# Kernel tuning notes

Measured on AMD Instinct MI355X. Metric: run time of the kernel, lower is better.

Reference implementation:

```python
import jax, jax.numpy as jnp
import numpy as np

NUM_FEATURES = 129  # lstm_hidden + 1
GAMMA = 1.0


def _lstm(x, W_ih, W_hh, b_ih, b_hh):
    # x: [B,S,F]; W_ih: [4H,F]; W_hh: [4H,H]; gates in torch order i,f,g,o
    B, S, _ = x.shape
    H = W_hh.shape[1]
    xg = jnp.einsum('bsf,gf->bsg', x, W_ih) + b_ih  # [B,S,4H]

    def step(carry, xt):
        h, c = carry
        g = xt + h @ W_hh.T + b_hh
        i, f, gg, o = jnp.split(g, 4, axis=-1)
        c = jax.nn.sigmoid(f) * c + jax.nn.sigmoid(i) * jnp.tanh(gg)
        h = jax.nn.sigmoid(o) * jnp.tanh(c)
        return (h, c), h

    h0 = jnp.zeros((B, H), x.dtype)
    (_, _), hs = jax.lax.scan(step, (h0, h0), jnp.swapaxes(xg, 0, 1))
    return jnp.swapaxes(hs, 0, 1)  # [B,S,H]


def setup_inputs() -> dict:
    key = jax.random.key(0)
    ks = jax.random.split(key, 10)
    B, S, F, H = 16, 2048, 129, 128
    s = 0.05  # keep activations in a sane range
    return {
        'x': jax.random.normal(ks[0], (B, S, F), jnp.float32),
        'prototypes': jax.random.normal(ks[1], (B, S, F), jnp.float32),
        'W_ih': jax.random.normal(ks[2], (4 * H, F), jnp.float32) * s,
        'W_hh': jax.random.normal(ks[3], (4 * H, H), jnp.float32) * s,
        'b_ih': jax.random.normal(ks[4], (4 * H,), jnp.float32) * s,
        'b_hh': jax.random.normal(ks[5], (4 * H,), jnp.float32) * s,
        'Wc': jax.random.normal(ks[6], (4, F, F), jnp.float32) * s,
        'bc': jax.random.normal(ks[7], (4, F), jnp.float32) * s,
        'Wh': jax.random.normal(ks[8], (2, F), jnp.float32) * s,
        'bh': jax.random.normal(ks[9], (2,), jnp.float32) * s,
    }


def reference(x, prototypes, W_ih, W_hh, b_ih, b_hh, Wc, bc, Wh, bh):
    lstm_out = _lstm(x, W_ih, W_hh, b_ih, b_hh)  # [B,S,H]
    # attention path is detached in the original (numpy round-trip)
    q = jax.lax.stop_gradient(lstm_out)
    # note: scale uses num_features (embed_dim of the attention object), not H
    scores = jnp.einsum('bqh,bkh->bqk', q, q) / jnp.sqrt(jnp.float32(NUM_FEATURES))
    attn = jax.nn.softmax(scores, axis=-1)
    context = jnp.einsum('bqk,bkh->bqh', attn, q)  # [B,S,H]
    # vectorized RBF kernel vs prototypes (original does a Python loop per (i,j))
    diff = x - prototypes
    kernel_features = jnp.exp(-GAMMA * jnp.sum(diff * diff, axis=-1, keepdims=True))  # [B,S,1]
    h = jnp.concatenate([context, kernel_features], axis=-1)  # [B,S,NUM_FEATURES]
    for l in range(4):
        h = jax.nn.relu(h @ Wc[l].T + bc[l])
    logits = h @ Wh.T + bh  # [B,S,2]
    return jax.nn.log_softmax(logits, axis=-1)
```

## Files before the change

kernel.cpp:

```cpp
#include <hip/hip_runtime.h>
#include <stdint.h>

#define B_ 16
#define S_ 2048
#define F_ 129
#define H_ 128
#define G_ 512

typedef float f32x4 __attribute__((ext_vector_type(4)));
typedef float f32x4a4 __attribute__((ext_vector_type(4), aligned(4)));
typedef float f32x2 __attribute__((ext_vector_type(2)));
typedef short s16x8 __attribute__((ext_vector_type(8)));
typedef _Float16 f16x8 __attribute__((ext_vector_type(8)));
typedef _Float16 f16x4 __attribute__((ext_vector_type(4)));

#define BAR_LDS() __asm__ volatile("s_waitcnt lgkmcnt(0)\n\ts_barrier" ::: "memory")

__device__ inline unsigned short h2bits(_Float16 h) {
  union { _Float16 h; unsigned short u; } v; v.h = h; return v.u;
}
__device__ inline unsigned short f2h(float f) { return h2bits((_Float16)f); }

__device__ inline float rcp_(float x) { return __builtin_amdgcn_rcpf(x); }

__device__ inline float sigmoid_fast(float x) { return rcp_(1.f + __expf(-x)); }

__device__ inline float tanh_fast(float x) {
  return 1.f - 2.f * rcp_(1.f + __expf(2.f * x));
}

__global__ __launch_bounds__(256) void xg_kernel(const float* __restrict__ x,
    const float* __restrict__ W_ih, const float* __restrict__ b_ih,
    const float* __restrict__ b_hh, _Float16* __restrict__ xg) {
  __shared__ __align__(16) _Float16 xs[64][136];
  __shared__ __align__(16) _Float16 ws[128][136];
  __shared__ float bsum[512];
  int tid = threadIdx.x;
  int lane = tid & 63, w = tid >> 6;
  int l15 = lane & 15, q = lane >> 4;
  long R0 = (long)blockIdx.x * 64;
  for (int it = 0; it < 8; ++it) {
    int i = tid + it * 256;
    int r = i >> 5, cx = (i & 31) * 4;
    f32x4a4 v = *(const f32x4a4*)&x[(R0 + r) * 129 + cx];
    f16x4 hq;
    #pragma unroll
    for (int j = 0; j < 4; ++j) hq[j] = (_Float16)v[j];
    *(f16x4*)&xs[r][cx] = hq;
  }
  if (tid < 64) xs[tid][128] = (_Float16)x[(R0 + tid) * 129 + 128];
  for (int it = 0; it < 2; ++it) {
    int g = tid + it * 256;
    bsum[g] = b_ih[g] + b_hh[g];
  }
  __syncthreads();
  f16x8 Bf[4];
  #pragma unroll
  for (int kb = 0; kb < 4; ++kb)
    Bf[kb] = *(const f16x8*)&xs[16 * w + l15][kb * 32 + q * 8];
  float x128 = (float)xs[16 * w + l15][128];
  f16x4 res[32];
  #pragma unroll
  for (int c = 0; c < 4; ++c) {
    __syncthreads();
    for (int it = 0; it < 16; ++it) {
      int i = tid + it * 256;
      int r = i >> 5, cc = (i & 31) * 4;
      f32x4a4 v = *(const f32x4a4*)&W_ih[(long)(c * 128 + r) * 129 + cc];
      f16x4 hq;
      #pragma unroll
      for (int j = 0; j < 4; ++j) hq[j] = (_Float16)v[j];
      *(f16x4*)&ws[r][cc] = hq;
    }
    if (tid < 128) ws[tid][128] = (_Float16)W_ih[(long)(c * 128 + tid) * 129 + 128];
    __syncthreads();
    #pragma unroll
    for (int t = 0; t < 8; ++t) {
      f32x4 acc;
      acc[0] = 0.f; acc[1] = 0.f; acc[2] = 0.f; acc[3] = 0.f;
      #pragma unroll
      for (int kb = 0; kb < 4; ++kb) {
        f16x8 Af = *(const f16x8*)&ws[t * 16 + l15][kb * 32 + q * 8];
        acc = __builtin_amdgcn_mfma_f32_16x16x32_f16(Af, Bf[kb], acc, 0, 0, 0);
      }
      #pragma unroll
      for (int r = 0; r < 4; ++r) {
        int unit = t * 16 + q * 4 + r;
        float v = acc[r] + bsum[c * 128 + unit] + x128 * (float)ws[unit][128];
        res[t * 4 + r][c] = (_Float16)v;
      }
    }
  }
  long rowbase = (R0 + 16 * w + l15) * G_;
  #pragma unroll
  for (int t = 0; t < 8; ++t)
    #pragma unroll
    for (int r = 0; r < 4; ++r)
      *(f16x4*)&xg[rowbase + (t * 16 + q * 4 + r) * 4] = res[t * 4 + r];
}

__global__ __launch_bounds__(256) void rbf_kernel(const float* __restrict__ x,
    const float* __restrict__ p, float* __restrict__ kf) {
  int wave = threadIdx.x >> 6, lane = threadIdx.x & 63;
  long row = (long)blockIdx.x * 4 + wave;
  const float* xr = x + row * F_;
  const float* pr = p + row * F_;
  float ss = 0.f;
  for (int k = lane; k < F_; k += 64) { float d = xr[k] - pr[k]; ss += d * d; }
  #pragma unroll
  for (int off = 32; off; off >>= 1) ss += __shfl_xor(ss, off, 64);
  if (lane == 0) kf[row] = __expf(-ss);
}

__global__ __launch_bounds__(512, 2) void lstm_kernel(const _Float16* __restrict__ xg,
    const float* __restrict__ W_hh, unsigned short* __restrict__ qbf) {
  __shared__ __align__(16) _Float16 hbuf[2][4 * 144];
  int tid = threadIdx.x;
  int w = tid >> 6, lane = tid & 63;
  int n16 = lane & 15;
  int q8 = lane >> 4;
  int ab = n16 >> 2;
  int u = (w << 4) | n16;
  int bb = blockIdx.x * 4;
  f16x8 Wf[4][4];
  #pragma unroll
  for (int ty = 0; ty < 4; ++ty) {
    #pragma unroll
    for (int kb = 0; kb < 4; ++kb) {
      const float* src = &W_hh[(ty * 128 + u) * H_ + kb * 32 + q8 * 8];
      f16x8 v;
      #pragma unroll
      for (int j = 0; j < 8; ++j) v[j] = (_Float16)src[j];
      Wf[ty][kb] = v;
    }
  }
  for (int i = tid; i < 2 * 4 * 144; i += 512)
    ((_Float16*)hbuf)[i] = (_Float16)0.f;
  float c = 0.f;
  int hoff = ab * 144 + q8 * 8;
  const _Float16* h0 = &hbuf[0][hoff];
  const _Float16* h1 = &hbuf[1][hoff];
  _Float16* hw = &hbuf[0][q8 * 144 + u];
  const int hstride = 4 * 144;
  const _Float16* xb = xg + (long)(bb + q8) * S_ * G_ + u * 4;
  unsigned short* qp = qbf + (long)(bb + q8) * S_ * H_ + u - H_;
  const _Float16* xpf = xb + 4 * G_;
  f16x4 cur[4];
  #pragma unroll
  for (int p = 0; p < 4; ++p) cur[p] = *(const f16x4*)(xb + (long)p * G_);
  unsigned short hvp = 0;
  __syncthreads();
  for (int t = 0; t < S_; t += 4) {
    #pragma unroll
    for (int p = 0; p < 4; ++p) {
      BAR_LDS();
      const _Float16* hsrc = (p & 1) ? h0 : h1;
      f16x8 A[4];
      #pragma unroll
      for (int kb = 0; kb < 4; ++kb)
        A[kb] = *(const f16x8*)(hsrc + kb * 32);
      if (t + p > 0)
        *qp = hvp;
      qp += H_;
      f16x4 xcur = cur[p];
      cur[p] = *(const f16x4*)xpf;
      xpf += G_;
      f32x4 r0a[4], r1a[4];
      #pragma unroll
      for (int ty = 0; ty < 4; ++ty) {
        f32x4 a0, a1;
        a0[0] = (float)xcur[ty]; a0[1] = 0.f; a0[2] = 0.f; a0[3] = 0.f;
        a1[0] = 0.f; a1[1] = 0.f; a1[2] = 0.f; a1[3] = 0.f;
        a0 = __builtin_amdgcn_mfma_f32_16x16x32_f16(A[0], Wf[ty][0], a0, 0, 0, 0);
        a1 = __builtin_amdgcn_mfma_f32_16x16x32_f16(A[2], Wf[ty][2], a1, 0, 0, 0);
        a0 = __builtin_amdgcn_mfma_f32_16x16x32_f16(A[1], Wf[ty][1], a0, 0, 0, 0);
        a1 = __builtin_amdgcn_mfma_f32_16x16x32_f16(A[3], Wf[ty][3], a1, 0, 0, 0);
        r0a[ty] = a0; r1a[ty] = a1;
      }
      float g0 = r0a[0][0] + r1a[0][0];
      float g1 = r0a[1][0] + r1a[1][0];
      float g2 = r0a[2][0] + r1a[2][0];
      float g3 = r0a[3][0] + r1a[3][0];
      float ai = sigmoid_fast(g0);
      float af = sigmoid_fast(g1);
      float ag = tanh_fast(g2);
      float ao = sigmoid_fast(g3);
      c = af * c + ai * ag;
      float hv = ao * tanh_fast(c);
      _Float16 hf = (_Float16)hv;
      hw[(p & 1) * hstride] = hf;
      hvp = h2bits(hf);
    }
  }
  *qp = hvp;
}

__global__ __launch_bounds__(256) void attn_kernel(const unsigned short* __restrict__ qbf,
    float* __restrict__ ctx) {
  __shared__ __align__(16) unsigned short Ks[64 * 136];
  __shared__ __align__(16) unsigned short VT[128 * 72];
  __shared__ __align__(16) unsigned short Ps[4 * 16 * 72];
  int tid = threadIdx.x;
  int lane = tid & 63, w = tid >> 6;
  int b = blockIdx.x >> 5;
  int q0 = (blockIdx.x & 31) * 64;
  const unsigned short* qb = qbf + (long)b * S_ * H_;
  int l15 = lane & 15;
  int koff = (lane >> 4) * 8;
  f16x8 qfrag[4];
  #pragma unroll
  for (int kb = 0; kb < 4; ++kb)
    qfrag[kb] = *(const f16x8*)(qb + (long)(q0 + w * 16 + l15) * H_ + kb * 32 + koff);
  f32x4 oacc[8];
  #pragma unroll
  for (int n = 0; n < 8; ++n)
    #pragma unroll
    for (int r = 0; r < 4; ++r) oacc[n][r] = 0.f;
  float mrow[4], lrow[4];
  #pragma unroll
  for (int r = 0; r < 4; ++r) { mrow[r] = -1e30f; lrow[r] = 0.f; }
  const float scale = 0.08804509063256238f;
  unsigned short* Pw = &Ps[w * 16 * 72];
  for (int t = 0; t < S_ / 64; ++t) {
    {
      int rr = tid >> 4;
      int c0 = (tid & 15) * 8;
      #pragma unroll
      for (int pch = 0; pch < 4; ++pch) {
        int r = pch * 16 + rr;
        s16x8 v = *(const s16x8*)(qb + (long)(t * 64 + r) * H_ + c0);
        *(s16x8*)(&Ks[r * 136 + c0]) = v;
        int rbase = r >> 3, rl = r & 7;
        #pragma unroll
        for (int i = 0; i < 8; ++i) {
          int d = c0 + i;
          VT[d * 72 + ((rbase ^ ((d >> 3) & 7)) << 3) + rl] = (unsigned short)v[i];
        }
      }
    }
    __syncthreads();
    f32x4 sacc[4];
    #pragma unroll
    for (int n = 0; n < 4; ++n) {
      f32x4 acc;
      #pragma unroll
      for (int r = 0; r < 4; ++r) acc[r] = 0.f;
      #pragma unroll
      for (int kb = 0; kb < 4; ++kb) {
        f16x8 bfrag = *(const f16x8*)(&Ks[(n * 16 + l15) * 136 + kb * 32 + koff]);
        acc = __builtin_amdgcn_mfma_f32_16x16x32_f16(qfrag[kb], bfrag, acc, 0, 0, 0);
      }
      sacc[n] = acc;
    }
    #pragma unroll
    for (int r = 0; r < 4; ++r) {
      float mx = fmaxf(fmaxf(sacc[0][r], sacc[1][r]), fmaxf(sacc[2][r], sacc[3][r]));
      #pragma unroll
      for (int m = 1; m < 16; m <<= 1) mx = fmaxf(mx, __shfl_xor(mx, m, 64));
      mx *= scale;
      float mnew = fmaxf(mrow[r], mx);
      float alpha = __expf(mrow[r] - mnew);
      mrow[r] = mnew;
      float psum = 0.f;
      #pragma unroll
      for (int n = 0; n < 4; ++n) {
        float pv = __expf(sacc[n][r] * scale - mnew);
        sacc[n][r] = pv;
        psum += pv;
      }
      #pragma unroll
      for (int m = 1; m < 16; m <<= 1) psum += __shfl_xor(psum, m, 64);
      lrow[r] = lrow[r] * alpha + psum;
      #pragma unroll
      for (int n = 0; n < 8; ++n) oacc[n][r] *= alpha;
    }
    #pragma unroll
    for (int n = 0; n < 4; ++n)
      #pragma unroll
      for (int r = 0; r < 4; ++r)
        Pw[((lane >> 4) * 4 + r) * 72 + n * 16 + l15] = f2h(sacc[n][r]);
    __syncthreads();
    #pragma unroll
    for (int kb = 0; kb < 2; ++kb) {
      f16x8 afrag = *(const f16x8*)(&Pw[l15 * 72 + kb * 32 + koff]);
      #pragma unroll
      for (int n = 0; n < 8; ++n) {
        int d = n * 16 + l15;
        int rb = ((kb * 32 + koff) >> 3) ^ ((d >> 3) & 7);
        f16x8 bfrag = *(const f16x8*)(&VT[d * 72 + (rb << 3)]);
        oacc[n] = __builtin_amdgcn_mfma_f32_16x16x32_f16(afrag, bfrag, oacc[n], 0, 0, 0);
      }
    }
    __syncthreads();
  }
  float* cb = ctx + (long)b * S_ * H_;
  #pragma unroll
  for (int n = 0; n < 8; ++n)
    #pragma unroll
    for (int r = 0; r < 4; ++r) {
      int row = q0 + w * 16 + (lane >> 4) * 4 + r;
      cb[(long)row * H_ + n * 16 + l15] = oacc[n][r] / lrow[r];
    }
}

__global__ __launch_bounds__(256) void mlp_kernel(const float* __restrict__ ctx,
    const float* __restrict__ kf, const float* __restrict__ Wc,
    const float* __restrict__ bc, const float* __restrict__ Wh,
    const float* __restrict__ bh, float* __restrict__ out) {
  __shared__ __align__(16) _Float16 hb[2][64][136];
  __shared__ __align__(16) _Float16 wl[144][136];
  __shared__ float bl[144];
  int tid = threadIdx.x;
  int lane = tid & 63, w = tid >> 6;
  int l15 = lane & 15, q = lane >> 4;
  long R0 = (long)blockIdx.x * 64;
  for (int it = 0; it < 8; ++it) {
    int i = tid + it * 256;
    int r = i >> 5, cx = (i & 31) * 4;
    f32x4 v = *(const f32x4*)&ctx[(R0 + r) * H_ + cx];
    f16x4 hq;
    #pragma unroll
    for (int j = 0; j < 4; ++j) hq[j] = (_Float16)v[j];
    *(f16x4*)&hb[0][r][cx] = hq;
  }
  if (tid < 64) hb[0][tid][128] = (_Float16)kf[R0 + tid];
  int cur = 0;
  for (int l = 0; l < 4; ++l) {
    __syncthreads();
    for (int it = 0; it < 18; ++it) {
      int i = tid + it * 256;
      int r = i >> 5, cc = (i & 31) * 4;
      int rs = (r < 129) ? r : 128;
      f32x4a4 v = *(const f32x4a4*)&Wc[((long)l * 129 + rs) * 129 + cc];
      f16x4 hq;
      #pragma unroll
      for (int j = 0; j < 4; ++j) hq[j] = (_Float16)v[j];
      *(f16x4*)&wl[r][cc] = hq;
    }
    if (tid < 144) {
      int rs = (tid < 129) ? tid : 128;
      wl[tid][128] = (_Float16)Wc[((long)l * 129 + rs) * 129 + 128];
      bl[tid] = bc[l * 129 + rs];
    }
    __syncthreads();
    f16x8 Bf[4];
    #pragma unroll
    for (int kb = 0; kb < 4; ++kb)
      Bf[kb] = *(const f16x8*)&hb[cur][16 * w + l15][kb * 32 + q * 8];
    float h128 = (float)hb[cur][16 * w + l15][128];
    int nxt = cur ^ 1;
    #pragma unroll
    for (int t = 0; t < 9; ++t) {
      f32x4 acc;
      acc[0] = 0.f; acc[1] = 0.f; acc[2] = 0.f; acc[3] = 0.f;
      #pragma unroll
      for (int kb = 0; kb < 4; ++kb) {
        f16x8 Af = *(const f16x8*)&wl[t * 16 + l15][kb * 32 + q * 8];
        acc = __builtin_amdgcn_mfma_f32_16x16x32_f16(Af, Bf[kb], acc, 0, 0, 0);
      }
      f16x4 hv;
      #pragma unroll
      for (int r = 0; r < 4; ++r) {
        int u = t * 16 + q * 4 + r;
        float v = acc[r] + bl[u] + h128 * (float)wl[u][128];
        hv[r] = (_Float16)fmaxf(v, 0.f);
      }
      if (t < 8)
        *(f16x4*)&hb[nxt][16 * w + l15][t * 16 + q * 4] = hv;
      else if (q == 0)
        hb[nxt][16 * w + l15][128] = hv[0];
    }
    cur ^= 1;
  }
  __syncthreads();
  if (tid < 128) {
    int row = tid >> 1, j = tid & 1;
    float z = bh[j];
    const float* whp = Wh + j * 129;
    for (int k = 0; k < 129; ++k) z += (float)hb[cur][row][k] * whp[k];
    float zo = __shfl_xor(z, 1, 64);
    float mx = fmaxf(z, zo);
    float lse = mx + __logf(__expf(z - mx) + __expf(zo - mx));
    out[(R0 + row) * 2 + j] = z - lse;
  }
}

extern "C" void kernel_launch(void* const* d_in, const int* in_sizes, int n_in,
                              void* d_out, int out_size, void* d_ws, size_t ws_size,
                              hipStream_t stream) {
  const float* x    = (const float*)d_in[0];
  const float* prot = (const float*)d_in[1];
  const float* W_ih = (const float*)d_in[2];
  const float* W_hh = (const float*)d_in[3];
  const float* b_ih = (const float*)d_in[4];
  const float* b_hh = (const float*)d_in[5];
  const float* Wc   = (const float*)d_in[6];
  const float* bc   = (const float*)d_in[7];
  const float* Wh   = (const float*)d_in[8];
  const float* bh   = (const float*)d_in[9];
  float* out = (float*)d_out;
  char* ws = (char*)d_ws;
  _Float16* xgh       = (_Float16*)(ws);
  unsigned short* qbf = (unsigned short*)(ws + 33554432);
  float* kf           = (float*)(ws + 41943040);
  float* ctx          = (float*)(ws + 42074112);

  hipLaunchKernelGGL(xg_kernel,  dim3(512),  dim3(256), 0, stream, x, W_ih, b_ih, b_hh, xgh);
  hipLaunchKernelGGL(rbf_kernel, dim3(8192), dim3(256), 0, stream, x, prot, kf);
  hipLaunchKernelGGL(lstm_kernel, dim3(4),   dim3(512), 0, stream, xgh, W_hh, qbf);
  hipLaunchKernelGGL(attn_kernel, dim3(512), dim3(256), 0, stream, qbf, ctx);
  hipLaunchKernelGGL(mlp_kernel,  dim3(512), dim3(256), 0, stream, ctx, kf, Wc, bc, Wh, bh, out);
}
```

Measured before the change: 1.153 ms.

## Overlap LSTM recurrence with input projection via progress flags and fuse attention into MLP

Merges the input-gate projection, RBF and LSTM kernels into one persistent launch. The four LSTM blocks spin on per-chunk atomic progress counters, so the recurrence can start once the first 64-step chunks of xg are written, instead of waiting for the whole projection. Gate scaling by log2(e) is folded into W_ih, W_hh and the biases so each activation uses a raw v_exp_f32. The attention output now goes straight into the MLP's shared memory in fp16, which removes the fp32 ctx round-trip through global memory and one launch. The spin-waits assume the producer blocks are scheduled alongside the LSTM blocks, which risks deadlock or stalls if the LSTM blocks occupy CUs first and starve the producers.

```diff
diff --git a/kernel.cpp b/kernel.cpp
--- a/kernel.cpp
+++ b/kernel.cpp
@@ -9,204 +9,236 @@
 
 typedef float f32x4 __attribute__((ext_vector_type(4)));
 typedef float f32x4a4 __attribute__((ext_vector_type(4), aligned(4)));
-typedef float f32x2 __attribute__((ext_vector_type(2)));
 typedef short s16x8 __attribute__((ext_vector_type(8)));
 typedef _Float16 f16x8 __attribute__((ext_vector_type(8)));
 typedef _Float16 f16x4 __attribute__((ext_vector_type(4)));
 
 #define BAR_LDS() __asm__ volatile("s_waitcnt lgkmcnt(0)\n\ts_barrier" ::: "memory")
+
+#define L2E 1.44269504088896f
 
 __device__ inline unsigned short h2bits(_Float16 h) {
   union { _Float16 h; unsigned short u; } v; v.h = h; return v.u;
 }
 __device__ inline unsigned short f2h(float f) { return h2bits((_Float16)f); }
-
 __device__ inline float rcp_(float x) { return __builtin_amdgcn_rcpf(x); }
-
-__device__ inline float sigmoid_fast(float x) { return rcp_(1.f + __expf(-x)); }
-
-__device__ inline float tanh_fast(float x) {
-  return 1.f - 2.f * rcp_(1.f + __expf(2.f * x));
+__device__ inline float exp2_(float x) {
+  float r; __asm__("v_exp_f32 %0, %1" : "=v"(r) : "v"(x)); return r;
 }
 
-__global__ __launch_bounds__(256) void xg_kernel(const float* __restrict__ x,
-    const float* __restrict__ W_ih, const float* __restrict__ b_ih,
-    const float* __restrict__ b_hh, _Float16* __restrict__ xg) {
-  __shared__ __align__(16) _Float16 xs[64][136];
-  __shared__ __align__(16) _Float16 ws[128][136];
-  __shared__ float bsum[512];
+__global__ __launch_bounds__(512, 2) void front_kernel(
+    const float* __restrict__ x, const float* __restrict__ prot,
+    const float* __restrict__ W_ih, const float* __restrict__ W_hh,
+    const float* __restrict__ b_ih, const float* __restrict__ b_hh,
+    _Float16* __restrict__ xg, unsigned short* __restrict__ qbf,
+    float* __restrict__ kf, int* __restrict__ prog) {
+  __shared__ __align__(16) char smem[82048];
   int tid = threadIdx.x;
-  int lane = tid & 63, w = tid >> 6;
-  int l15 = lane & 15, q = lane >> 4;
-  long R0 = (long)blockIdx.x * 64;
-  for (int it = 0; it < 8; ++it) {
-    int i = tid + it * 256;
-    int r = i >> 5, cx = (i & 31) * 4;
-    f32x4a4 v = *(const f32x4a4*)&x[(R0 + r) * 129 + cx];
-    f16x4 hq;
-    #pragma unroll
-    for (int j = 0; j < 4; ++j) hq[j] = (_Float16)v[j];
-    *(f16x4*)&xs[r][cx] = hq;
+  int blk = blockIdx.x;
+
+  if (blk < 4) {
+    _Float16 (*hbuf)[4 * 144] = (_Float16 (*)[4 * 144])smem;
+    int w = tid >> 6, lane = tid & 63;
+    int n16 = lane & 15;
+    int q8 = lane >> 4;
+    int ab = n16 >> 2;
+    int u = (w << 4) | n16;
+    int bb = blk * 4;
+    f16x8 Wf[4][4];
+    #pragma unroll
+    for (int ty = 0; ty < 4; ++ty) {
+      float gs = (ty == 2) ? (2.f * L2E) : (-L2E);
+      #pragma unroll
+      for (int kb = 0; kb < 4; ++kb) {
+        const float* src = &W_hh[(ty * 128 + u) * H_ + kb * 32 + q8 * 8];
+        f16x8 v;
+        #pragma unroll
+        for (int j = 0; j < 8; ++j) v[j] = (_Float16)(src[j] * gs);
+        Wf[ty][kb] = v;
+      }
+    }
+    for (int i = tid; i < 2 * 4 * 144; i += 512)
+      ((_Float16*)hbuf)[i] = (_Float16)0.f;
+    float c = 0.f;
+    int hoff = ab * 144 + q8 * 8;
+    const _Float16* h0 = &hbuf[0][hoff];
+    const _Float16* h1 = &hbuf[1][hoff];
+    _Float16* hw = &hbuf[0][q8 * 144 + u];
+    const int hstride = 4 * 144;
+    const _Float16* xb = xg + (long)(bb + q8) * S_ * G_ + u * 4;
+    unsigned short* qp = qbf + (long)(bb + q8) * S_ * H_ + u - H_;
+    const _Float16* xpf = xb + 4 * G_;
+    while (__hip_atomic_load(&prog[0], __ATOMIC_ACQUIRE, __HIP_MEMORY_SCOPE_AGENT) < 16)
+      __builtin_amdgcn_s_sleep(2);
+    while (__hip_atomic_load(&prog[1], __ATOMIC_ACQUIRE, __HIP_MEMORY_SCOPE_AGENT) < 16)
+      __builtin_amdgcn_s_sleep(2);
+    f16x4 cur[4];
+    #pragma unroll
+    for (int p = 0; p < 4; ++p) cur[p] = *(const f16x4*)(xb + (long)p * G_);
+    unsigned short hvp = 0;
+    __syncthreads();
+    for (int t = 0; t < S_; t += 4) {
+      if ((t & 63) == 0 && t != 0 && t < 1984) {
+        int cn = (t >> 6) + 1;
+        while (__hip_atomic_load(&prog[cn], __ATOMIC_ACQUIRE, __HIP_MEMORY_SCOPE_AGENT) < 16)
+          __builtin_amdgcn_s_sleep(2);
+      }
+      #pragma unroll
+      for (int p = 0; p < 4; ++p) {
+        BAR_LDS();
+        const _Float16* hsrc = (p & 1) ? h0 : h1;
+        f16x8 A[4];
+        #pragma unroll
+        for (int kb = 0; kb < 4; ++kb)
+          A[kb] = *(const f16x8*)(hsrc + kb * 32);
+        if (t + p > 0)
+          *qp = hvp;
+        qp += H_;
+        f16x4 xcur = cur[p];
+        cur[p] = *(const f16x4*)xpf;
+        xpf += G_;
+        f32x4 r0a[4], r1a[4];
+        #pragma unroll
+        for (int ty = 0; ty < 4; ++ty) {
+          f32x4 a0, a1;
+          a0[0] = (float)xcur[ty]; a0[1] = 0.f; a0[2] = 0.f; a0[3] = 0.f;
+          a1[0] = 0.f; a1[1] = 0.f; a1[2] = 0.f; a1[3] = 0.f;
+          a0 = __builtin_amdgcn_mfma_f32_16x16x32_f16(A[0], Wf[ty][0], a0, 0, 0, 0);
+          a1 = __builtin_amdgcn_mfma_f32_16x16x32_f16(A[2], Wf[ty][2], a1, 0, 0, 0);
+          a0 = __builtin_amdgcn_mfma_f32_16x16x32_f16(A[1], Wf[ty][1], a0, 0, 0, 0);
+          a1 = __builtin_amdgcn_mfma_f32_16x16x32_f16(A[3], Wf[ty][3], a1, 0, 0, 0);
+          r0a[ty] = a0; r1a[ty] = a1;
+        }
+        float g0 = r0a[0][0] + r1a[0][0];
+        float g1 = r0a[1][0] + r1a[1][0];
+        float g2 = r0a[2][0] + r1a[2][0];
+        float g3 = r0a[3][0] + r1a[3][0];
+        float ai = rcp_(1.f + exp2_(g0));
+        float af = rcp_(1.f + exp2_(g1));
+        float ag = 1.f - 2.f * rcp_(1.f + exp2_(g2));
+        float ao = rcp_(1.f + exp2_(g3));
+        c = af * c + ai * ag;
+        float th = 1.f - 2.f * rcp_(1.f + exp2_(c * (2.f * L2E)));
+        float hv = ao * th;
+        _Float16 hf = (_Float16)hv;
+        hw[(p & 1) * hstride] = hf;
+        hvp = h2bits(hf);
+      }
+    }
+    *qp = hvp;
+
+  } else if (blk < 516) {
+    _Float16 (*xs)[136] = (_Float16 (*)[136])smem;
+    _Float16 (*ws)[136] = (_Float16 (*)[136])(smem + 17408);
+    float* bsum = (float*)(smem + 17408 + 34816);
+    int xblk = blk - 4;
+    int batch = xblk & 15, chunk = xblk >> 4;
+    long R0 = (long)batch * S_ + chunk * 64;
+    int lane = tid & 63, w = tid >> 6;
+    int tw = w & 3, hi = w >> 2;
+    int l15 = lane & 15, q = lane >> 4;
+    for (int it = 0; it < 4; ++it) {
+      int i = tid + it * 512;
+      int r = i >> 5, cx = (i & 31) * 4;
+      f32x4a4 v = *(const f32x4a4*)&x[(R0 + r) * 129 + cx];
+      f16x4 hq;
+      #pragma unroll
+      for (int j = 0; j < 4; ++j) hq[j] = (_Float16)v[j];
+      *(f16x4*)&xs[r][cx] = hq;
+    }
+    if (tid < 64) xs[tid][128] = (_Float16)x[(R0 + tid) * 129 + 128];
+    bsum[tid] = b_ih[tid] + b_hh[tid];
+    __syncthreads();
+    f16x8 Bf[4];
+    #pragma unroll
+    for (int kb = 0; kb < 4; ++kb)
+      Bf[kb] = *(const f16x8*)&xs[16 * tw + l15][kb * 32 + q * 8];
+    float x128 = (float)xs[16 * tw + l15][128];
+    f16x4 res[16];
+    #pragma unroll
+    for (int cg = 0; cg < 4; ++cg) {
+      __syncthreads();
+      for (int it = 0; it < 8; ++it) {
+        int i = tid + it * 512;
+        int r = i >> 5, cc = (i & 31) * 4;
+        f32x4a4 v = *(const f32x4a4*)&W_ih[(long)(cg * 128 + r) * 129 + cc];
+        f16x4 hq;
+        #pragma unroll
+        for (int j = 0; j < 4; ++j) hq[j] = (_Float16)v[j];
+        *(f16x4*)&ws[r][cc] = hq;
+      }
+      if (tid < 128) ws[tid][128] = (_Float16)W_ih[(long)(cg * 128 + tid) * 129 + 128];
+      __syncthreads();
+      float gs = (cg == 2) ? (2.f * L2E) : (-L2E);
+      #pragma unroll
+      for (int t = 0; t < 4; ++t) {
+        int tt = hi * 4 + t;
+        f32x4 acc;
+        acc[0] = 0.f; acc[1] = 0.f; acc[2] = 0.f; acc[3] = 0.f;
+        #pragma unroll
+        for (int kb = 0; kb < 4; ++kb) {
+          f16x8 Af = *(const f16x8*)&ws[tt * 16 + l15][kb * 32 + q * 8];
+          acc = __builtin_amdgcn_mfma_f32_16x16x32_f16(Af, Bf[kb], acc, 0, 0, 0);
+        }
+        #pragma unroll
+        for (int r = 0; r < 4; ++r) {
+          int unit = tt * 16 + q * 4 + r;
+          float vv = (acc[r] + bsum[cg * 128 + unit] + x128 * (float)ws[unit][128]) * gs;
+          res[t * 4 + r][cg] = (_Float16)vv;
+        }
+      }
+    }
+    long rowbase = (R0 + 16 * tw + l15) * G_;
+    #pragma unroll
+    for (int t = 0; t < 4; ++t)
+      #pragma unroll
+      for (int r = 0; r < 4; ++r)
+        *(f16x4*)&xg[rowbase + ((hi * 4 + t) * 16 + q * 4 + r) * 4] = res[t * 4 + r];
+    __syncthreads();
+    if (tid == 0) {
+      __threadfence();
+      __hip_atomic_fetch_add(&prog[chunk], 1, __ATOMIC_RELEASE, __HIP_MEMORY_SCOPE_AGENT);
+    }
+
+  } else {
+    int rblk = blk - 516;
+    int wave = tid >> 6, lane = tid & 63;
+    for (int it = 0; it < 8; ++it) {
+      long row = (long)rblk * 64 + it * 8 + wave;
+      const float* xr = x + row * F_;
+      const float* pr = prot + row * F_;
+      float ss = 0.f;
+      for (int k = lane; k < F_; k += 64) { float d = xr[k] - pr[k]; ss += d * d; }
+      #pragma unroll
+      for (int off = 32; off; off >>= 1) ss += __shfl_xor(ss, off, 64);
+      if (lane == 0) kf[row] = __expf(-ss);
+    }
   }
-  if (tid < 64) xs[tid][128] = (_Float16)x[(R0 + tid) * 129 + 128];
-  for (int it = 0; it < 2; ++it) {
-    int g = tid + it * 256;
-    bsum[g] = b_ih[g] + b_hh[g];
-  }
-  __syncthreads();
-  f16x8 Bf[4];
-  #pragma unroll
-  for (int kb = 0; kb < 4; ++kb)
-    Bf[kb] = *(const f16x8*)&xs[16 * w + l15][kb * 32 + q * 8];
-  float x128 = (float)xs[16 * w + l15][128];
-  f16x4 res[32];
-  #pragma unroll
-  for (int c = 0; c < 4; ++c) {
-    __syncthreads();
-    for (int it = 0; it < 16; ++it) {
-      int i = tid + it * 256;
-      int r = i >> 5, cc = (i & 31) * 4;
-      f32x4a4 v = *(const f32x4a4*)&W_ih[(long)(c * 128 + r) * 129 + cc];
-      f16x4 hq;
-      #pragma unroll
-      for (int j = 0; j < 4; ++j) hq[j] = (_Float16)v[j];
-      *(f16x4*)&ws[r][cc] = hq;
-    }
-    if (tid < 128) ws[tid][128] = (_Float16)W_ih[(long)(c * 128 + tid) * 129 + 128];
-    __syncthreads();
-    #pragma unroll
-    for (int t = 0; t < 8; ++t) {
-      f32x4 acc;
-      acc[0] = 0.f; acc[1] = 0.f; acc[2] = 0.f; acc[3] = 0.f;
-      #pragma unroll
-      for (int kb = 0; kb < 4; ++kb) {
-        f16x8 Af = *(const f16x8*)&ws[t * 16 + l15][kb * 32 + q * 8];
-        acc = __builtin_amdgcn_mfma_f32_16x16x32_f16(Af, Bf[kb], acc, 0, 0, 0);
-      }
-      #pragma unroll
-      for (int r = 0; r < 4; ++r) {
-        int unit = t * 16 + q * 4 + r;
-        float v = acc[r] + bsum[c * 128 + unit] + x128 * (float)ws[unit][128];
-        res[t * 4 + r][c] = (_Float16)v;
-      }
-    }
-  }
-  long rowbase = (R0 + 16 * w + l15) * G_;
-  #pragma unroll
-  for (int t = 0; t < 8; ++t)
-    #pragma unroll
-    for (int r = 0; r < 4; ++r)
-      *(f16x4*)&xg[rowbase + (t * 16 + q * 4 + r) * 4] = res[t * 4 + r];
 }
 
-__global__ __launch_bounds__(256) void rbf_kernel(const float* __restrict__ x,
-    const float* __restrict__ p, float* __restrict__ kf) {
-  int wave = threadIdx.x >> 6, lane = threadIdx.x & 63;
-  long row = (long)blockIdx.x * 4 + wave;
-  const float* xr = x + row * F_;
-  const float* pr = p + row * F_;
-  float ss = 0.f;
-  for (int k = lane; k < F_; k += 64) { float d = xr[k] - pr[k]; ss += d * d; }
-  #pragma unroll
-  for (int off = 32; off; off >>= 1) ss += __shfl_xor(ss, off, 64);
-  if (lane == 0) kf[row] = __expf(-ss);
-}
-
-__global__ __launch_bounds__(512, 2) void lstm_kernel(const _Float16* __restrict__ xg,
-    const float* __restrict__ W_hh, unsigned short* __restrict__ qbf) {
-  __shared__ __align__(16) _Float16 hbuf[2][4 * 144];
-  int tid = threadIdx.x;
-  int w = tid >> 6, lane = tid & 63;
-  int n16 = lane & 15;
-  int q8 = lane >> 4;
-  int ab = n16 >> 2;
-  int u = (w << 4) | n16;
-  int bb = blockIdx.x * 4;
-  f16x8 Wf[4][4];
-  #pragma unroll
-  for (int ty = 0; ty < 4; ++ty) {
-    #pragma unroll
-    for (int kb = 0; kb < 4; ++kb) {
-      const float* src = &W_hh[(ty * 128 + u) * H_ + kb * 32 + q8 * 8];
-      f16x8 v;
-      #pragma unroll
-      for (int j = 0; j < 8; ++j) v[j] = (_Float16)src[j];
-      Wf[ty][kb] = v;
-    }
-  }
-  for (int i = tid; i < 2 * 4 * 144; i += 512)
-    ((_Float16*)hbuf)[i] = (_Float16)0.f;
-  float c = 0.f;
-  int hoff = ab * 144 + q8 * 8;
-  const _Float16* h0 = &hbuf[0][hoff];
-  const _Float16* h1 = &hbuf[1][hoff];
-  _Float16* hw = &hbuf[0][q8 * 144 + u];
-  const int hstride = 4 * 144;
-  const _Float16* xb = xg + (long)(bb + q8) * S_ * G_ + u * 4;
-  unsigned short* qp = qbf + (long)(bb + q8) * S_ * H_ + u - H_;
-  const _Float16* xpf = xb + 4 * G_;
-  f16x4 cur[4];
-  #pragma unroll
-  for (int p = 0; p < 4; ++p) cur[p] = *(const f16x4*)(xb + (long)p * G_);
-  unsigned short hvp = 0;
-  __syncthreads();
-  for (int t = 0; t < S_; t += 4) {
-    #pragma unroll
-    for (int p = 0; p < 4; ++p) {
-      BAR_LDS();
-      const _Float16* hsrc = (p & 1) ? h0 : h1;
-      f16x8 A[4];
-      #pragma unroll
-      for (int kb = 0; kb < 4; ++kb)
-        A[kb] = *(const f16x8*)(hsrc + kb * 32);
-      if (t + p > 0)
-        *qp = hvp;
-      qp += H_;
-      f16x4 xcur = cur[p];
-      cur[p] = *(const f16x4*)xpf;
-      xpf += G_;
-      f32x4 r0a[4], r1a[4];
-      #pragma unroll
-      for (int ty = 0; ty < 4; ++ty) {
-        f32x4 a0, a1;
-        a0[0] = (float)xcur[ty]; a0[1] = 0.f; a0[2] = 0.f; a0[3] = 0.f;
-        a1[0] = 0.f; a1[1] = 0.f; a1[2] = 0.f; a1[3] = 0.f;
-        a0 = __builtin_amdgcn_mfma_f32_16x16x32_f16(A[0], Wf[ty][0], a0, 0, 0, 0);
-        a1 = __builtin_amdgcn_mfma_f32_16x16x32_f16(A[2], Wf[ty][2], a1, 0, 0, 0);
-        a0 = __builtin_amdgcn_mfma_f32_16x16x32_f16(A[1], Wf[ty][1], a0, 0, 0, 0);
-        a1 = __builtin_amdgcn_mfma_f32_16x16x32_f16(A[3], Wf[ty][3], a1, 0, 0, 0);
-        r0a[ty] = a0; r1a[ty] = a1;
-      }
-      float g0 = r0a[0][0] + r1a[0][0];
-      float g1 = r0a[1][0] + r1a[1][0];
-      float g2 = r0a[2][0] + r1a[2][0];
-      float g3 = r0a[3][0] + r1a[3][0];
-      float ai = sigmoid_fast(g0);
-      float af = sigmoid_fast(g1);
-      float ag = tanh_fast(g2);
-      float ao = sigmoid_fast(g3);
-      c = af * c + ai * ag;
-      float hv = ao * tanh_fast(c);
-      _Float16 hf = (_Float16)hv;
-      hw[(p & 1) * hstride] = hf;
-      hvp = h2bits(hf);
-    }
-  }
-  *qp = hvp;
-}
-
-__global__ __launch_bounds__(256) void attn_kernel(const unsigned short* __restrict__ qbf,
-    float* __restrict__ ctx) {
-  __shared__ __align__(16) unsigned short Ks[64 * 136];
-  __shared__ __align__(16) unsigned short VT[128 * 72];
-  __shared__ __align__(16) unsigned short Ps[4 * 16 * 72];
+__global__ __launch_bounds__(256) void back_kernel(
+    const unsigned short* __restrict__ qbf, const float* __restrict__ kf,
+    const float* __restrict__ Wc, const float* __restrict__ bc,
+    const float* __restrict__ Wh, const float* __restrict__ bh,
+    float* __restrict__ out) {
+  __shared__ __align__(16) char smem[74560];
+  _Float16 (*hb)[64][136] = (_Float16 (*)[64][136])smem;
+  unsigned short* Ps = (unsigned short*)(smem + 17408);
+  unsigned short* Ks = (unsigned short*)(smem + 34816);
+  unsigned short* VT = (unsigned short*)(smem + 34816 + 17408);
+  _Float16 (*wl)[136] = (_Float16 (*)[136])(smem + 34816);
+  float* bl = (float*)(smem + 34816 + 39168);
+
   int tid = threadIdx.x;
   int lane = tid & 63, w = tid >> 6;
   int b = blockIdx.x >> 5;
   int q0 = (blockIdx.x & 31) * 64;
+  long R0 = (long)blockIdx.x * 64;
   const unsigned short* qb = qbf + (long)b * S_ * H_;
   int l15 = lane & 15;
-  int koff = (lane >> 4) * 8;
+  int q = lane >> 4;
+  int koff = q * 8;
+
   f16x8 qfrag[4];
   #pragma unroll
   for (int kb = 0; kb < 4; ++kb)
@@ -220,7 +252,7 @@
   #pragma unroll
   for (int r = 0; r < 4; ++r) { mrow[r] = -1e30f; lrow[r] = 0.f; }
   const float scale = 0.08804509063256238f;
-  unsigned short* Pw = &Ps[w * 16 * 72];
+  unsigned short* Pw = Ps + w * 16 * 72;
   for (int t = 0; t < S_ / 64; ++t) {
     {
       int rr = tid >> 4;
@@ -278,7 +310,7 @@
     for (int n = 0; n < 4; ++n)
       #pragma unroll
       for (int r = 0; r < 4; ++r)
-        Pw[((lane >> 4) * 4 + r) * 72 + n * 16 + l15] = f2h(sacc[n][r]);
+        Pw[(q * 4 + r) * 72 + n * 16 + l15] = f2h(sacc[n][r]);
     __syncthreads();
     #pragma unroll
     for (int kb = 0; kb < 2; ++kb) {
@@ -293,37 +325,16 @@
     }
     __syncthreads();
   }
-  float* cb = ctx + (long)b * S_ * H_;
+  float rl4[4];
+  #pragma unroll
+  for (int r = 0; r < 4; ++r) rl4[r] = rcp_(lrow[r]);
   #pragma unroll
   for (int n = 0; n < 8; ++n)
     #pragma unroll
-    for (int r = 0; r < 4; ++r) {
-      int row = q0 + w * 16 + (lane >> 4) * 4 + r;
-      cb[(long)row * H_ + n * 16 + l15] = oacc[n][r] / lrow[r];
-    }
-}
-
-__global__ __launch_bounds__(256) void mlp_kernel(const float* __restrict__ ctx,
-    const float* __restrict__ kf, const float* __restrict__ Wc,
-    const float* __restrict__ bc, const float* __restrict__ Wh,
-    const float* __restrict__ bh, float* __restrict__ out) {
-  __shared__ __align__(16) _Float16 hb[2][64][136];
-  __shared__ __align__(16) _Float16 wl[144][136];
-  __shared__ float bl[144];
-  int tid = threadIdx.x;
-  int lane = tid & 63, w = tid >> 6;
-  int l15 = lane & 15, q = lane >> 4;
-  long R0 = (long)blockIdx.x * 64;
-  for (int it = 0; it < 8; ++it) {
-    int i = tid + it * 256;
-    int r = i >> 5, cx = (i & 31) * 4;
-    f32x4 v = *(const f32x4*)&ctx[(R0 + r) * H_ + cx];
-    f16x4 hq;
-    #pragma unroll
-    for (int j = 0; j < 4; ++j) hq[j] = (_Float16)v[j];
-    *(f16x4*)&hb[0][r][cx] = hq;
-  }
+    for (int r = 0; r < 4; ++r)
+      hb[0][w * 16 + q * 4 + r][n * 16 + l15] = (_Float16)(oacc[n][r] * rl4[r]);
   if (tid < 64) hb[0][tid][128] = (_Float16)kf[R0 + tid];
+
   int cur = 0;
   for (int l = 0; l < 4; ++l) {
     __syncthreads();
@@ -403,11 +414,11 @@
   _Float16* xgh       = (_Float16*)(ws);
   unsigned short* qbf = (unsigned short*)(ws + 33554432);
   float* kf           = (float*)(ws + 41943040);
-  float* ctx          = (float*)(ws + 42074112);
-
-  hipLaunchKernelGGL(xg_kernel,  dim3(512),  dim3(256), 0, stream, x, W_ih, b_ih, b_hh, xgh);
-  hipLaunchKernelGGL(rbf_kernel, dim3(8192), dim3(256), 0, stream, x, prot, kf);
-  hipLaunchKernelGGL(lstm_kernel, dim3(4),   dim3(512), 0, stream, xgh, W_hh, qbf);
-  hipLaunchKernelGGL(attn_kernel, dim3(512), dim3(256), 0, stream, qbf, ctx);
-  hipLaunchKernelGGL(mlp_kernel,  dim3(512), dim3(256), 0, stream, ctx, kf, Wc, bc, Wh, bh, out);
+  int* prog           = (int*)(ws + 42074112);
+
+  hipMemsetAsync(prog, 0, 128, stream);
+  hipLaunchKernelGGL(front_kernel, dim3(1028), dim3(512), 0, stream,
+                     x, prot, W_ih, W_hh, b_ih, b_hh, xgh, qbf, kf, prog);
+  hipLaunchKernelGGL(back_kernel, dim3(512), dim3(256), 0, stream,
+                     qbf, kf, Wc, bc, Wh, bh, out);
 }
```

After: 1.131 ms. 2.0% less time.
